# Kernel optimization log

Hardware: AMD Instinct MI355X
Metric: run time of the kernel (lower is better)

The kernel has to match this reference:

```python
import jax, jax.numpy as jnp
import numpy as np

# Dimensions: B walkers, NSPIN spins, NPS electrons per spin, DFEAT equivariant
# feature dim, NION ions, DSP spatial dim.
B, NSPIN, NPS, DFEAT, NION, DSP = 2048, 2, 8, 256, 4, 3


def setup_inputs() -> dict:
    key = jax.random.key(0)
    k0, k1, k2, k3, k4, k5 = jax.random.split(key, 6)
    eq_inputs = jax.random.normal(k0, (B, NSPIN * NPS, DFEAT), jnp.float32)
    r_ei = jax.random.normal(k1, (B, NSPIN * NPS, NION, DSP), jnp.float32)
    # Linear part of the orbitals: maps pair features (2*DFEAT) -> NPS orbitals per spin.
    W = jax.random.normal(k2, (NSPIN, 2 * DFEAT, NPS), jnp.float32) / np.sqrt(2.0 * DFEAT)
    b = 0.01 * jax.random.normal(k3, (NSPIN, NPS), jnp.float32)
    # Anisotropic decay: one DSPxDSP matrix per (spin, orbital, ion), near identity.
    env_dim = jnp.eye(DSP, dtype=jnp.float32)[None, None, None] + 0.05 * jax.random.normal(
        k4, (NSPIN, NPS, NION, DSP, DSP), jnp.float32
    )
    # Linear combination over ions per (spin, ion, orbital).
    env_ion = jnp.full((NSPIN, NION, NPS), 1.0 / NION, jnp.float32) + 0.05 * jax.random.normal(
        k5, (NSPIN, NION, NPS), jnp.float32
    )
    return {
        "eq_inputs": eq_inputs,
        "r_ei": r_ei,
        "W": W,
        "b": b,
        "env_dim": env_dim,
        "env_ion": env_ion,
    }


def reference(eq_inputs, r_ei, W, b, env_dim, env_ion):
    Bsz = eq_inputs.shape[0]
    # Split equally into spins: (B, NSPIN, NPS, DFEAT)
    x = eq_inputs.reshape(Bsz, NSPIN, NPS, DFEAT)
    # Doubly-equivariant pair features: concat(x_i, x_j) -> (B, S, n, n, 2d)
    shp = (Bsz, NSPIN, NPS, NPS, DFEAT)
    xi = jnp.broadcast_to(x[:, :, :, None, :], shp)
    xj = jnpp_concat = jnp.broadcast_to(x[:, :, None, :, :], shp)
    pairs = jnp.concatenate([xi, xj], axis=-1)
    # Linear part of the per-particle orbital matrices: (B, S, i, j, k)
    orb = jnp.einsum("bsijf,sfk->bsijk", pairs, W) + b[None, :, None, None, :]
    # Anisotropic exponential envelopes on the orbital-evaluated electron j:
    # env_{b,s,j,k} = sum_a env_ion[s,a,k] * exp(-||env_dim[s,k,a] @ r_ei[b,s,j,a]||)
    r = r_ei.reshape(Bsz, NSPIN, NPS, NION, DSP)
    scaled = jnp.einsum("bsjad,skade->bsjkae", r, env_dim)  # (B,S,j,k,a,e)
    dist = jnp.linalg.norm(scaled, axis=-1)  # (B,S,j,k,a)
    env = jnp.einsum("bsjka,sak->bsjk", jnp.exp(-dist), env_ion)
    orb = orb * env[:, :, None, :, :]
    # Per-particle determinants over the (j,k) axes: (B, S, n)
    dets = jnp.linalg.det(orb)[..., None]  # (B, S, n, 1)
    # Per-spin list, each (B, n, 1)
    return (dets[:, 0], dets[:, 1])
```

## Files before the change

### kernel.cpp

```cpp
#include <hip/hip_runtime.h>
#include <stdint.h>

#define BATCH 2048
#define NPS 8
#define DFEAT 256

typedef const float __attribute__((address_space(4))) cfp;
typedef __attribute__((address_space(3))) uint32_t lds_u32;
typedef const __attribute__((address_space(1))) uint32_t glb_u32;

__global__ __launch_bounds__(512) void ppdet_kernel(
    const float* __restrict__ eq,
    const float* __restrict__ r_ei,
    const float* __restrict__ W,
    const float* __restrict__ bias,
    const float* __restrict__ env_dim,
    const float* __restrict__ env_ion,
    float* __restrict__ out)
{
    __shared__ __align__(16) float X[64 * DFEAT];
    __shared__ __align__(16) float AB[64 * 16];
    __shared__ __align__(16) float envl[512];
    float* part = X;

    const int tid = threadIdx.x;
    const int bid = blockIdx.x;
    const int s  = bid & 1;
    const int b0 = (bid >> 1) * 8;

    const int wq   = __builtin_amdgcn_readfirstlane(tid >> 6);
    const int lane = tid & 63;

    {
        const float* gbase = eq + ((size_t)(b0 + wq) * 16 + s * 8) * DFEAT;
#pragma unroll
        for (int u = 0; u < 8; ++u) {
            const float* src = gbase + u * DFEAT + ((lane ^ u) << 2);
            lds_u32* dst = (lds_u32*)(uintptr_t)(&X[(wq * 8 + u) * DFEAT]);
            __builtin_amdgcn_global_load_lds((glb_u32*)src, dst, 16, 0, 0);
        }
    }

    {
        const int w = tid >> 6, k = (tid >> 3) & 7, j = tid & 7;
        const size_t rrow = ((size_t)(b0 + w) * 16 + s * 8 + j) * 12;
        const float4* rp = (const float4*)(r_ei + rrow);
        float4 ra = rp[0], rb = rp[1], rc = rp[2];
        float rr[12] = {ra.x, ra.y, ra.z, ra.w, rb.x, rb.y, rb.z, rb.w,
                        rc.x, rc.y, rc.z, rc.w};
        float e = 0.f;
#pragma unroll
        for (int a = 0; a < 4; ++a) {
            const float* Md = env_dim + ((size_t)(s * 8 + k) * 4 + a) * 9;
            float r0 = rr[a * 3], r1 = rr[a * 3 + 1], r2 = rr[a * 3 + 2];
            float e0 = r0 * Md[0] + r1 * Md[3] + r2 * Md[6];
            float e1 = r0 * Md[1] + r1 * Md[4] + r2 * Md[7];
            float e2 = r0 * Md[2] + r1 * Md[5] + r2 * Md[8];
            float dist = sqrtf(e0 * e0 + e1 * e1 + e2 * e2);
            e = fmaf(env_ion[(s * 4 + a) * 8 + k], __expf(-dist), e);
        }
        envl[w * 64 + j * 8 + k] = e;
    }

    __syncthreads();

    float4 xv[8];
    {
        const int swz = lane & 7;
#pragma unroll
        for (int j = 0; j < 8; ++j) {
            const int c16 = (wq * 8 + j) ^ swz;
            xv[j] = *(const float4*)&X[lane * DFEAT + c16 * 4];
        }
    }

    float acc[16];
#pragma unroll
    for (int k = 0; k < 16; ++k) acc[k] = 0.f;

    cfp* wb1 = (cfp*)(uintptr_t)(W + s * 4096 + wq * 256);
#pragma unroll
    for (int u = 0; u < 8; ++u) {
        cfp* wr = wb1 + u * 32;
        float xs0 = xv[u].x, xs1 = xv[u].y, xs2 = xv[u].z, xs3 = xv[u].w;
#pragma unroll
        for (int c = 0; c < 4; ++c) {
            float xc = (c == 0) ? xs0 : (c == 1) ? xs1 : (c == 2) ? xs2 : xs3;
#pragma unroll
            for (int k = 0; k < 8; ++k) {
                acc[k]     = fmaf(xc, wr[c * 8 + k],        acc[k]);
                acc[8 + k] = fmaf(xc, wr[2048 + c * 8 + k], acc[8 + k]);
            }
        }
    }

    __syncthreads();

    {
        float* pb = part + (wq * 64 + lane) * 16;
        const int sw = (lane >> 1) & 3;
#pragma unroll
        for (int kg = 0; kg < 4; ++kg) {
            int slot = kg ^ sw;
            float4 v = make_float4(acc[kg * 4], acc[kg * 4 + 1],
                                   acc[kg * 4 + 2], acc[kg * 4 + 3]);
            *(float4*)(pb + slot * 4) = v;
        }
    }

    __syncthreads();

    if (tid < 256) {
        const int row = tid >> 2, sl = tid & 3;
        const int g = sl ^ ((row >> 1) & 3);
        float4 sum = make_float4(0.f, 0.f, 0.f, 0.f);
#pragma unroll
        for (int q2 = 0; q2 < 8; ++q2) {
            float4 v = *(const float4*)(part + (q2 * 64 + row) * 16 + sl * 4);
            sum.x += v.x; sum.y += v.y; sum.z += v.z; sum.w += v.w;
        }
        if (g < 2) {
            sum.x += bias[s * 8 + g * 4];
            sum.y += bias[s * 8 + g * 4 + 1];
            sum.z += bias[s * 8 + g * 4 + 2];
            sum.w += bias[s * 8 + g * 4 + 3];
        }
        *(float4*)(AB + row * 16 + g * 4) = sum;
    }

    __syncthreads();

    if (tid < 64) {
        const int w = tid >> 3, i = tid & 7;
        float Arow[8];
#pragma unroll
        for (int k = 0; k < 8; ++k) Arow[k] = AB[(w * 8 + i) * 16 + k];
        float M[8][8];
#pragma unroll
        for (int j = 0; j < 8; ++j) {
#pragma unroll
            for (int k = 0; k < 8; ++k)
                M[j][k] = (Arow[k] + AB[(w * 8 + j) * 16 + 8 + k])
                          * envl[w * 64 + j * 8 + k];
        }
        float det = 1.f;
#pragma unroll
        for (int p = 0; p < 8; ++p) {
            int piv = p;
            float mx = fabsf(M[p][p]);
#pragma unroll
            for (int r2 = p + 1; r2 < 8; ++r2) {
                float v = fabsf(M[r2][p]);
                if (v > mx) { mx = v; piv = r2; }
            }
#pragma unroll
            for (int r2 = p + 1; r2 < 8; ++r2) {
                bool sw = (piv == r2);
#pragma unroll
                for (int c = p; c < 8; ++c) {
                    float a = M[p][c], bb = M[r2][c];
                    M[p][c]  = sw ? bb : a;
                    M[r2][c] = sw ? a : bb;
                }
            }
            det = (piv != p) ? -det : det;
            float d = M[p][p];
            det *= d;
            float inv = (d != 0.f) ? 1.f / d : 0.f;
#pragma unroll
            for (int r2 = p + 1; r2 < 8; ++r2) {
                float fct = M[r2][p] * inv;
#pragma unroll
                for (int c = p + 1; c < 8; ++c) M[r2][c] -= fct * M[p][c];
            }
        }
        out[(size_t)s * (BATCH * NPS) + (size_t)(b0 + w) * NPS + i] = det;
    }
}

extern "C" void kernel_launch(void* const* d_in, const int* in_sizes, int n_in,
                              void* d_out, int out_size, void* d_ws, size_t ws_size,
                              hipStream_t stream) {
    const float* eq      = (const float*)d_in[0];
    const float* r_ei    = (const float*)d_in[1];
    const float* W       = (const float*)d_in[2];
    const float* bias    = (const float*)d_in[3];
    const float* env_dim = (const float*)d_in[4];
    const float* env_ion = (const float*)d_in[5];
    float* out = (float*)d_out;

    ppdet_kernel<<<512, 512, 0, stream>>>(eq, r_ei, W, bias, env_dim, env_ion, out);
}
```

Measured before the change: 15.52 us.

## Pipeline feature loads in four column chunks overlapped with partial matmul

The eq tile is now loaded into LDS as four 64-column chunks, each with its own swizzle. Staged s_waitcnt vmcnt plus barriers let each wave start the W-projection FMAs on chunk q while later chunks are still in flight. The envelope computation moves after the matmul and partial-sum store, which also removes one block-wide sync. The gain is overlap of global-memory latency with compute. The cost is four barriers and hand-coded vmcnt counts, which depend on no other vector-memory ops being interleaved.

```diff
diff --git a/kernel.cpp b/kernel.cpp
--- a/kernel.cpp
+++ b/kernel.cpp
@@ -18,7 +18,7 @@
     const float* __restrict__ env_ion,
     float* __restrict__ out)
 {
-    __shared__ __align__(16) float X[64 * DFEAT];
+    __shared__ __align__(16) float X[4 * 64 * 64];
     __shared__ __align__(16) float AB[64 * 16];
     __shared__ __align__(16) float envl[512];
     float* part = X;
@@ -32,12 +32,64 @@
     const int lane = tid & 63;
 
     {
-        const float* gbase = eq + ((size_t)(b0 + wq) * 16 + s * 8) * DFEAT;
+        const float* gw = eq + ((size_t)(b0 + wq) * 16 + s * 8) * DFEAT;
 #pragma unroll
-        for (int u = 0; u < 8; ++u) {
-            const float* src = gbase + u * DFEAT + ((lane ^ u) << 2);
-            lds_u32* dst = (lds_u32*)(uintptr_t)(&X[(wq * 8 + u) * DFEAT]);
-            __builtin_amdgcn_global_load_lds((glb_u32*)src, dst, 16, 0, 0);
+        for (int q = 0; q < 4; ++q) {
+#pragma unroll
+            for (int u = 0; u < 2; ++u) {
+                const int r0 = wq * 8 + u * 4;
+                const int r  = r0 + (lane >> 4);
+                const int c  = (lane & 15) ^ ((r >> 1) & 7);
+                const float* src = gw + (size_t)(r & 7) * DFEAT + q * 64 + c * 4;
+                lds_u32* dst = (lds_u32*)(uintptr_t)&X[q * 4096 + r0 * 64];
+                __builtin_amdgcn_global_load_lds((glb_u32*)src, dst, 16, 0, 0);
+            }
+            __builtin_amdgcn_sched_barrier(0);
+        }
+    }
+
+    float acc[16];
+#pragma unroll
+    for (int k = 0; k < 16; ++k) acc[k] = 0.f;
+
+    cfp* wbase = (cfp*)(uintptr_t)(W + s * 4096);
+    const int perm = (lane >> 1) & 7;
+
+#pragma unroll
+    for (int q = 0; q < 4; ++q) {
+        if (q == 0)      asm volatile("s_waitcnt vmcnt(6)" ::: "memory");
+        else if (q == 1) asm volatile("s_waitcnt vmcnt(4)" ::: "memory");
+        else if (q == 2) asm volatile("s_waitcnt vmcnt(2)" ::: "memory");
+        else             asm volatile("s_waitcnt vmcnt(0)" ::: "memory");
+        __builtin_amdgcn_s_barrier();
+        __builtin_amdgcn_sched_barrier(0);
+
+        const float4 xa = *(const float4*)
+            &X[q * 4096 + lane * 64 + (((2 * wq)     ^ perm) << 2)];
+        const float4 xb = *(const float4*)
+            &X[q * 4096 + lane * 64 + (((2 * wq + 1) ^ perm) << 2)];
+        cfp* w1 = wbase + (q * 64 + wq * 8) * 8;
+        const float xs[8] = {xa.x, xa.y, xa.z, xa.w, xb.x, xb.y, xb.z, xb.w};
+#pragma unroll
+        for (int i = 0; i < 8; ++i) {
+            const float xc = xs[i];
+#pragma unroll
+            for (int k = 0; k < 8; ++k) {
+                acc[k]     = fmaf(xc, w1[i * 8 + k],        acc[k]);
+                acc[8 + k] = fmaf(xc, w1[2048 + i * 8 + k], acc[8 + k]);
+            }
+        }
+    }
+
+    {
+        float* pb = part + (wq * 64 + lane) * 16;
+        const int sw = (lane >> 1) & 3;
+#pragma unroll
+        for (int kg = 0; kg < 4; ++kg) {
+            int slot = kg ^ sw;
+            float4 v = make_float4(acc[kg * 4], acc[kg * 4 + 1],
+                                   acc[kg * 4 + 2], acc[kg * 4 + 3]);
+            *(float4*)(pb + slot * 4) = v;
         }
     }
 
@@ -60,52 +112,6 @@
             e = fmaf(env_ion[(s * 4 + a) * 8 + k], __expf(-dist), e);
         }
         envl[w * 64 + j * 8 + k] = e;
-    }
-
-    __syncthreads();
-
-    float4 xv[8];
-    {
-        const int swz = lane & 7;
-#pragma unroll
-        for (int j = 0; j < 8; ++j) {
-            const int c16 = (wq * 8 + j) ^ swz;
-            xv[j] = *(const float4*)&X[lane * DFEAT + c16 * 4];
-        }
-    }
-
-    float acc[16];
-#pragma unroll
-    for (int k = 0; k < 16; ++k) acc[k] = 0.f;
-
-    cfp* wb1 = (cfp*)(uintptr_t)(W + s * 4096 + wq * 256);
-#pragma unroll
-    for (int u = 0; u < 8; ++u) {
-        cfp* wr = wb1 + u * 32;
-        float xs0 = xv[u].x, xs1 = xv[u].y, xs2 = xv[u].z, xs3 = xv[u].w;
-#pragma unroll
-        for (int c = 0; c < 4; ++c) {
-            float xc = (c == 0) ? xs0 : (c == 1) ? xs1 : (c == 2) ? xs2 : xs3;
-#pragma unroll
-            for (int k = 0; k < 8; ++k) {
-                acc[k]     = fmaf(xc, wr[c * 8 + k],        acc[k]);
-                acc[8 + k] = fmaf(xc, wr[2048 + c * 8 + k], acc[8 + k]);
-            }
-        }
-    }
-
-    __syncthreads();
-
-    {
-        float* pb = part + (wq * 64 + lane) * 16;
-        const int sw = (lane >> 1) & 3;
-#pragma unroll
-        for (int kg = 0; kg < 4; ++kg) {
-            int slot = kg ^ sw;
-            float4 v = make_float4(acc[kg * 4], acc[kg * 4 + 1],
-                                   acc[kg * 4 + 2], acc[kg * 4 + 3]);
-            *(float4*)(pb + slot * 4) = v;
-        }
     }
 
     __syncthreads();
```

Result: faster. 14.98 us (-3.5%).
